# Kernel optimization log

Measured on AMD Instinct MI355X. Metric: run time of the kernel, lower is better.

## Reference

```python
import jax, jax.numpy as jnp
import numpy as np
import math

B, T, D = 2, 2048, 2048
H, HKV = 32, 8
DH = D // H          # 64
G = H // HKV         # 4 query heads per kv head
ROPE_BASE = 10000.0


def _rope_cos_sin(t, dh):
    inv_freq = 1.0 / (ROPE_BASE ** (jnp.arange(0, dh, 2, dtype=jnp.float32) / dh))
    pos = jnp.arange(t, dtype=jnp.float32)
    freqs = pos[:, None] * inv_freq[None, :]          # [T, Dh/2]
    emb = jnp.concatenate([freqs, freqs], axis=-1)    # [T, Dh]
    return jnp.cos(emb), jnp.sin(emb)


def _rotate_half(y):
    y1, y2 = jnp.split(y, 2, axis=-1)
    return jnp.concatenate([-y2, y1], axis=-1)


def _apply_rope(x, cos, sin):  # x: [..., T, Dh]; cos/sin: [T, Dh]
    return x * cos + _rotate_half(x) * sin


def setup_inputs() -> dict:
    key = jax.random.key(0)
    k = jax.random.split(key, 5)
    x = jax.random.normal(k[0], (B, T, D), dtype=jnp.float32)
    Wq = jax.random.normal(k[1], (D, D), dtype=jnp.float32) * 0.02
    Wk = jax.random.normal(k[2], (D, HKV * DH), dtype=jnp.float32) * 0.02
    Wv = jax.random.normal(k[3], (D, HKV * DH), dtype=jnp.float32) * 0.02
    Wo = jax.random.normal(k[4], (D, D), dtype=jnp.float32) * 0.02
    causal = jnp.tril(jnp.ones((T, T), dtype=bool))
    attn_mask = jnp.where(causal, 0.0, -1e9).astype(jnp.float32)[None, None]  # [1,1,T,T]
    return {"x": x, "Wq": Wq, "Wk": Wk, "Wv": Wv, "Wo": Wo, "attn_mask": attn_mask}


def reference(x, Wq, Wk, Wv, Wo, attn_mask):
    Bx, Tx, Dx = x.shape
    # projections (Linear, no bias)
    q = (x @ Wq).reshape(Bx, Tx, H, DH).transpose(0, 2, 1, 3)      # [B,H,T,Dh]
    kk = (x @ Wk).reshape(Bx, Tx, HKV, DH).transpose(0, 2, 1, 3)   # [B,Hkv,T,Dh]
    vv = (x @ Wv).reshape(Bx, Tx, HKV, DH).transpose(0, 2, 1, 3)   # [B,Hkv,T,Dh]
    # RoPE on q and k (offset=0, no kv cache)
    cos, sin = _rope_cos_sin(Tx, DH)
    q = _apply_rope(q, cos, sin)
    kk = _apply_rope(kk, cos, sin)
    # GQA: group query heads so head h uses kv head h // G (matches repeat_interleave)
    qg = q.reshape(Bx, HKV, G, Tx, DH)
    att = jnp.einsum('bkgtd,bksd->bkgts', qg, kk) / math.sqrt(DH)
    att = att + attn_mask[:, :, None]                              # broadcast over groups
    p = jax.nn.softmax(att, axis=-1)
    ctx = jnp.einsum('bkgts,bksd->bkgtd', p, vv)                   # [B,Hkv,G,T,Dh]
    ctx = ctx.reshape(Bx, H, Tx, DH).transpose(0, 2, 1, 3).reshape(Bx, Tx, Dx)
    return ctx @ Wo
```

## Files before the change

kernel.cpp:

```cpp
#include <hip/hip_runtime.h>
#include <hip/hip_bf16.h>


typedef __bf16 bf16_t;
typedef __bf16 bf16x4 __attribute__((ext_vector_type(4)));
typedef __bf16 bf16x8 __attribute__((ext_vector_type(8)));
typedef float f32x4 __attribute__((ext_vector_type(4)));

#define B_ 2
#define T_ 2048
#define D_ 2048
#define H_ 32
#define HKV_ 8
#define DH_ 64

__device__ __forceinline__ float fast_exp2(float x) { return __builtin_amdgcn_exp2f(x); }

__device__ __forceinline__ void gld_lds16(const bf16_t* g, bf16_t* l) {
  __builtin_amdgcn_global_load_lds((const __attribute__((address_space(1))) unsigned int*)g,
                                   (__attribute__((address_space(3))) unsigned int*)l, 16, 0, 0);
}

__global__ __launch_bounds__(256) void cast_f32_bf16(const float* __restrict__ in,
                                                     bf16_t* __restrict__ out, int n) {
  int i = (blockIdx.x * 256 + threadIdx.x) * 8;
  if (i < n) {
    f32x4 a = *(const f32x4*)&in[i];
    f32x4 b = *(const f32x4*)&in[i + 4];
    bf16x8 o;
    o[0] = (bf16_t)a[0]; o[1] = (bf16_t)a[1]; o[2] = (bf16_t)a[2]; o[3] = (bf16_t)a[3];
    o[4] = (bf16_t)b[0]; o[5] = (bf16_t)b[1]; o[6] = (bf16_t)b[2]; o[7] = (bf16_t)b[3];
    *(bf16x8*)&out[i] = o;
  }
}

__global__ __launch_bounds__(256) void transpose_w(const float* __restrict__ W,
                                                   bf16_t* __restrict__ Wt, int K, int N) {
  __shared__ float tile[64][65];
  int n0 = blockIdx.x * 64, k0 = blockIdx.y * 64;
  int tid = threadIdx.x;
  for (int i = tid; i < 4096; i += 256) {
    int r = i >> 6, c = i & 63;
    tile[r][c] = W[(size_t)(k0 + r) * N + n0 + c];
  }
  __syncthreads();
  for (int i = tid; i < 4096; i += 256) {
    int r = i >> 6, c = i & 63;
    Wt[(size_t)(n0 + r) * K + k0 + c] = (bf16_t)tile[c][r];
  }
}

__global__ __launch_bounds__(256) void transpose_wqkv(const float* __restrict__ Wq,
                                                      const float* __restrict__ Wk,
                                                      const float* __restrict__ Wv,
                                                      bf16_t* __restrict__ Wt) {
  __shared__ float tile[64][65];
  int n0 = blockIdx.x * 64, k0 = blockIdx.y * 64;
  const float* W;
  int srcN, col;
  if (n0 < 2048) { W = Wq; srcN = 2048; col = n0; }
  else if (n0 < 2560) { W = Wk; srcN = 512; col = n0 - 2048; }
  else { W = Wv; srcN = 512; col = n0 - 2560; }
  int tid = threadIdx.x;
  for (int i = tid; i < 4096; i += 256) {
    int r = i >> 6, c = i & 63;
    tile[r][c] = W[(size_t)(k0 + r) * srcN + col + c];
  }
  __syncthreads();
  for (int i = tid; i < 4096; i += 256) {
    int r = i >> 6, c = i & 63;
    Wt[(size_t)(n0 + r) * 2048 + k0 + c] = (bf16_t)tile[c][r];
  }
}

template <typename OutT>
__global__ __launch_bounds__(256) void gemm_bt(const bf16_t* __restrict__ A,
                                               const bf16_t* __restrict__ Bt,
                                               OutT* __restrict__ C, int M, int N, int K) {
  __shared__ __align__(16) bf16_t As[2 * 128 * 32];
  __shared__ __align__(16) bf16_t Bs[2 * 128 * 32];
  int tid = threadIdx.x;
  int lane = tid & 63;
  int wave = tid >> 6;
  int l15 = lane & 15;
  int quad = lane >> 4;
  int m0 = blockIdx.y * 128;
  int n0 = blockIdx.x * 128;
  int wrow = (wave >> 1) * 64;
  int wcol = (wave & 1) * 64;

  f32x4 acc[4][4] = {};

  for (int kc = 0; kc < K; kc += 64) {
#pragma unroll
    for (int kk = 0; kk < 2; ++kk) {
#pragma unroll
      for (int c = 0; c < 2; ++c) {
        int linear = c * 256 + tid;
        int r = linear >> 2, seg = linear & 3;
        gld_lds16(&A[(size_t)(m0 + r) * K + kc + kk * 32 + seg * 8],
                  &As[kk * 4096 + (size_t)(c * 256 + wave * 64) * 8]);
        gld_lds16(&Bt[(size_t)(n0 + r) * K + kc + kk * 32 + seg * 8],
                  &Bs[kk * 4096 + (size_t)(c * 256 + wave * 64) * 8]);
      }
    }
    __syncthreads();
#pragma unroll
    for (int kk = 0; kk < 2; ++kk) {
      bf16x8 af[4], bfr[4];
#pragma unroll
      for (int mi = 0; mi < 4; ++mi)
        af[mi] = *(const bf16x8*)&As[kk * 4096 + (wrow + mi * 16 + l15) * 32 + quad * 8];
#pragma unroll
      for (int ni = 0; ni < 4; ++ni)
        bfr[ni] = *(const bf16x8*)&Bs[kk * 4096 + (wcol + ni * 16 + l15) * 32 + quad * 8];
#pragma unroll
      for (int mi = 0; mi < 4; ++mi)
#pragma unroll
        for (int ni = 0; ni < 4; ++ni)
          acc[mi][ni] = __builtin_amdgcn_mfma_f32_16x16x32_bf16(af[mi], bfr[ni], acc[mi][ni], 0, 0, 0);
    }
    __syncthreads();
  }
#pragma unroll
  for (int mi = 0; mi < 4; ++mi) {
#pragma unroll
    for (int ni = 0; ni < 4; ++ni) {
#pragma unroll
      for (int r = 0; r < 4; ++r) {
        int m = m0 + wrow + mi * 16 + quad * 4 + r;
        int n = n0 + wcol + ni * 16 + l15;
        C[(size_t)m * N + n] = (OutT)acc[mi][ni][r];
      }
    }
  }
}

__global__ __launch_bounds__(256) void rope_qk(const bf16_t* __restrict__ qkv,
                                               bf16_t* __restrict__ qr,
                                               bf16_t* __restrict__ kr) {
  int t = blockIdx.x, b = blockIdx.y;
  int tid = threadIdx.x;
  const bf16_t* row = qkv + (size_t)(b * T_ + t) * 3072;
  const float LN1E4_over32 = 9.210340371976184f / 32.0f;
  const float QSC = 1.44269504088896f * 0.125f;
  for (int i = tid; i < 1024 + 256; i += 256) {
    bool isq = i < 1024;
    int ii = isq ? i : i - 1024;
    int hh = ii >> 5, j = ii & 31;
    int base = isq ? 0 : 2048;
    float inv = __expf(-(float)j * LN1E4_over32);
    float fr = (float)t * inv;
    float sn, cs;
    sincosf(fr, &sn, &cs);
    float x1 = (float)row[base + hh * 64 + j];
    float x2 = (float)row[base + hh * 64 + j + 32];
    float o1 = x1 * cs - x2 * sn;
    float o2 = x2 * cs + x1 * sn;
    if (isq) {
      size_t o = ((size_t)(b * H_ + hh) * T_ + t) * DH_;
      qr[o + j] = (bf16_t)(o1 * QSC);
      qr[o + j + 32] = (bf16_t)(o2 * QSC);
    } else {
      size_t o = ((size_t)(b * HKV_ + hh) * T_ + t) * DH_;
      kr[o + j] = (bf16_t)o1;
      kr[o + j + 32] = (bf16_t)o2;
    }
  }
}

__global__ __launch_bounds__(256) void transpose_v(const bf16_t* __restrict__ qkv,
                                                   bf16_t* __restrict__ vtr) {
  __shared__ __align__(16) bf16_t tile[64][72];
  int t0 = blockIdx.x * 64;
  int hk = blockIdx.y;
  int b = blockIdx.z;
  int tid = threadIdx.x;
  for (int i = tid; i < 512; i += 256) {
    int r = i >> 3, s = i & 7;
    *(bf16x8*)&tile[r][s * 8] =
        *(const bf16x8*)&qkv[(size_t)(b * T_ + t0 + r) * 3072 + 2560 + hk * 64 + s * 8];
  }
  __syncthreads();
  for (int i = tid; i < 4096; i += 256) {
    int dd = i >> 6, tt = i & 63;
    vtr[((size_t)(b * HKV_ + hk) * DH_ + dd) * T_ + t0 + tt] = tile[tt][dd];
  }
}

#define DO_HALF(HALF, QF, O, LACC, DOMASK)                                             \
  {                                                                                    \
    f32x4 s_[4] = {};                                                                  \
    _Pragma("unroll") for (int mt = 0; mt < 4; ++mt) {                                 \
      bf16x8 ak0 = *(const bf16x8*)&Ks[(mt * 16 + l15) * 72 + quad * 8];               \
      bf16x8 ak1 = *(const bf16x8*)&Ks[(mt * 16 + l15) * 72 + 32 + quad * 8];          \
      s_[mt] = __builtin_amdgcn_mfma_f32_16x16x32_bf16(ak0, QF[0], s_[mt], 0, 0, 0);   \
      s_[mt] = __builtin_amdgcn_mfma_f32_16x16x32_bf16(ak1, QF[1], s_[mt], 0, 0, 0);   \
    }                                                                                  \
    if (DOMASK) {                                                                      \
      _Pragma("unroll") for (int mt = 0; mt < 4; ++mt)                                 \
          _Pragma("unroll") for (int r = 0; r < 4; ++r) if (mt * 16 + quad * 4 + r >   \
                                                            wave * 16 + l15)           \
              s_[mt][r] = -1e30f;                                                      \
    }                                                                                  \
    _Pragma("unroll") for (int mt = 0; mt < 4; ++mt) {                                 \
      bf16x4 pv;                                                                       \
      _Pragma("unroll") for (int r = 0; r < 4; ++r) {                                  \
        float p = fast_exp2(s_[mt][r]);                                                \
        LACC += p;                                                                     \
        pv[r] = (bf16_t)p;                                                             \
      }                                                                                \
      *(bf16x4*)&Ps[wave][HALF][l15 * 72 + mt * 16 + quad * 4] = pv;                   \
    }                                                                                  \
    _Pragma("unroll") for (int k0 = 0; k0 < 2; ++k0) {                                 \
      bf16x8 ap = *(const bf16x8*)&Ps[wave][HALF][l15 * 72 + k0 * 32 + quad * 8];      \
      _Pragma("unroll") for (int dn = 0; dn < 4; ++dn) {                               \
        bf16x8 bv = *(const bf16x8*)&Vt[(dn * 16 + l15) * 72 + k0 * 32 + quad * 8];    \
        O[dn] = __builtin_amdgcn_mfma_f32_16x16x32_bf16(ap, bv, O[dn], 0, 0, 0);       \
      }                                                                                \
    }                                                                                  \
  }

__global__ __launch_bounds__(256) void flash_attn(const bf16_t* __restrict__ qr,
                                                  const bf16_t* __restrict__ kr,
                                                  const bf16_t* __restrict__ vtr,
                                                  bf16_t* __restrict__ ctxb) {
  __shared__ __align__(16) bf16_t Ks[64 * 72];
  __shared__ __align__(16) bf16_t Vt[64 * 72];
  __shared__ __align__(16) bf16_t Ps[4][2][16 * 72];
  int tid = threadIdx.x;
  int lane = tid & 63;
  int wave = tid >> 6;
  int l15 = lane & 15, quad = lane >> 4;
  int pair = blockIdx.x, h = blockIdx.y, b = blockIdx.z;
  int qtA = pair, qtB = 31 - pair;
  int nkvA = qtA + 1, nkvB = qtB + 1;
  int kvh = h >> 2;

  const bf16_t* qbA = qr + ((size_t)(b * H_ + h) * T_ + qtA * 64 + wave * 16) * DH_;
  const bf16_t* qbB = qr + ((size_t)(b * H_ + h) * T_ + qtB * 64 + wave * 16) * DH_;
  const bf16_t* kbase = kr + (size_t)(b * HKV_ + kvh) * T_ * DH_;
  const bf16_t* vbase = vtr + (size_t)(b * HKV_ + kvh) * DH_ * T_;

  bf16x8 qA[2], qB[2];
#pragma unroll
  for (int k0 = 0; k0 < 2; ++k0) {
    qA[k0] = *(const bf16x8*)&qbA[l15 * 64 + k0 * 32 + quad * 8];
    qB[k0] = *(const bf16x8*)&qbB[l15 * 64 + k0 * 32 + quad * 8];
  }

  f32x4 oA[4] = {}, oB[4] = {};
  float lA = 0.f, lB = 0.f;

  bf16x8 kreg[2], vreg[2];
  auto load_kv = [&](int kv) {
#pragma unroll
    for (int c = 0; c < 2; ++c) {
      int idx = c * 256 + tid;
      int r = idx >> 3, sg = idx & 7;
      kreg[c] = *(const bf16x8*)&kbase[(size_t)kv * 4096 + r * 64 + sg * 8];
      vreg[c] = *(const bf16x8*)&vbase[(size_t)r * T_ + kv * 64 + sg * 8];
    }
  };
  load_kv(0);

  for (int kv = 0; kv < nkvB; ++kv) {
#pragma unroll
    for (int c = 0; c < 2; ++c) {
      int idx = c * 256 + tid;
      int r = idx >> 3, sg = idx & 7;
      *(bf16x8*)&Ks[r * 72 + sg * 8] = kreg[c];
      *(bf16x8*)&Vt[r * 72 + sg * 8] = vreg[c];
    }
    __syncthreads();
    if (kv + 1 < nkvB) load_kv(kv + 1);

    DO_HALF(1, qB, oB, lB, kv == qtB);
    if (kv < nkvA) DO_HALF(0, qA, oA, lA, kv == qtA);
    __syncthreads();
  }

  lA += __shfl_xor(lA, 16, 64);
  lA += __shfl_xor(lA, 32, 64);
  lB += __shfl_xor(lB, 16, 64);
  lB += __shfl_xor(lB, 32, 64);
  float invA = 1.0f / lA, invB = 1.0f / lB;
#pragma unroll
  for (int r = 0; r < 4; ++r) {
    float iAr = __shfl(invA, quad * 4 + r, 64);
    float iBr = __shfl(invB, quad * 4 + r, 64);
    int tA = qtA * 64 + wave * 16 + quad * 4 + r;
    int tB = qtB * 64 + wave * 16 + quad * 4 + r;
#pragma unroll
    for (int dn = 0; dn < 4; ++dn) {
      ctxb[(size_t)(b * T_ + tA) * D_ + h * 64 + dn * 16 + l15] = (bf16_t)(oA[dn][r] * iAr);
      ctxb[(size_t)(b * T_ + tB) * D_ + h * 64 + dn * 16 + l15] = (bf16_t)(oB[dn][r] * iBr);
    }
  }
}

extern "C" void kernel_launch(void* const* d_in, const int* in_sizes, int n_in,
                              void* d_out, int out_size, void* d_ws, size_t ws_size,
                              hipStream_t stream) {
  const float* x = (const float*)d_in[0];
  const float* Wq = (const float*)d_in[1];
  const float* Wk = (const float*)d_in[2];
  const float* Wv = (const float*)d_in[3];
  const float* Wo = (const float*)d_in[4];
  float* out = (float*)d_out;

  char* ws = (char*)d_ws;
  size_t off = 0;
  bf16_t* xb = (bf16_t*)(ws + off); off += (size_t)B_ * T_ * D_ * 2;
  bf16_t* wqkvb = (bf16_t*)(ws + off); off += (size_t)3072 * 2048 * 2;
  bf16_t* wob = (bf16_t*)(ws + off); off += (size_t)2048 * 2048 * 2;
  bf16_t* qkv = (bf16_t*)(ws + off); off += (size_t)4096 * 3072 * 2;
  bf16_t* qr = (bf16_t*)(ws + off); off += (size_t)B_ * H_ * T_ * DH_ * 2;
  bf16_t* kr = (bf16_t*)(ws + off); off += (size_t)B_ * HKV_ * T_ * DH_ * 2;
  bf16_t* vtr = (bf16_t*)(ws + off); off += (size_t)B_ * HKV_ * T_ * DH_ * 2;
  bf16_t* ctxb = (bf16_t*)(ws + off); off += (size_t)B_ * T_ * D_ * 2;

  int nx = B_ * T_ * D_;
  cast_f32_bf16<<<nx / 8 / 256, 256, 0, stream>>>(x, xb, nx);
  transpose_wqkv<<<dim3(3072 / 64, 2048 / 64), 256, 0, stream>>>(Wq, Wk, Wv, wqkvb);
  transpose_w<<<dim3(2048 / 64, 2048 / 64), 256, 0, stream>>>(Wo, wob, 2048, 2048);

  gemm_bt<bf16_t><<<dim3(3072 / 128, 4096 / 128), 256, 0, stream>>>(xb, wqkvb, qkv, 4096, 3072, 2048);

  rope_qk<<<dim3(T_, B_), 256, 0, stream>>>(qkv, qr, kr);
  transpose_v<<<dim3(T_ / 64, HKV_, B_), 256, 0, stream>>>(qkv, vtr);

  flash_attn<<<dim3(16, H_, B_), 256, 0, stream>>>(qr, kr, vtr, ctxb);

  gemm_bt<float><<<dim3(2048 / 128, 4096 / 128), 256, 0, stream>>>(ctxb, wob, out, 4096, 2048, 2048);
}
```

Before: 341.0 us.

## Keep P in registers via permuted V layout and double-buffer K/V LDS

The V transpose now writes keys in a permuted order that matches the MFMA accumulator layout of the score tile. This lets the attention kernel pack exp(S) directly into the A-operand registers for the PV MFMA, with no round trip through LDS. It also double-buffers the K/V shared tiles and drops the trailing barrier in each iteration, so fewer syncs are needed per KV step. The cost is twice the K/V LDS, plus reliance on a single barrier per iteration for correctness across buffers.

Result: faster. 317.3 us (-7.0%).

```diff
diff --git a/kernel.cpp b/kernel.cpp
--- a/kernel.cpp
+++ b/kernel.cpp
@@ -184,16 +184,17 @@
   __syncthreads();
   for (int i = tid; i < 4096; i += 256) {
     int dd = i >> 6, tt = i & 63;
-    vtr[((size_t)(b * HKV_ + hk) * DH_ + dd) * T_ + t0 + tt] = tile[tt][dd];
-  }
-}
-
-#define DO_HALF(HALF, QF, O, LACC, DOMASK)                                             \
+    int src = (tt & 32) | ((tt & 4) << 2) | ((tt & 24) >> 1) | (tt & 3);
+    vtr[((size_t)(b * HKV_ + hk) * DH_ + dd) * T_ + t0 + tt] = tile[src][dd];
+  }
+}
+
+#define DO_HALF(QF, O, LACC, DOMASK, KS, VT)                                           \
   {                                                                                    \
     f32x4 s_[4] = {};                                                                  \
     _Pragma("unroll") for (int mt = 0; mt < 4; ++mt) {                                 \
-      bf16x8 ak0 = *(const bf16x8*)&Ks[(mt * 16 + l15) * 72 + quad * 8];               \
-      bf16x8 ak1 = *(const bf16x8*)&Ks[(mt * 16 + l15) * 72 + 32 + quad * 8];          \
+      bf16x8 ak0 = *(const bf16x8*)&KS[(mt * 16 + l15) * 72 + quad * 8];               \
+      bf16x8 ak1 = *(const bf16x8*)&KS[(mt * 16 + l15) * 72 + 32 + quad * 8];          \
       s_[mt] = __builtin_amdgcn_mfma_f32_16x16x32_bf16(ak0, QF[0], s_[mt], 0, 0, 0);   \
       s_[mt] = __builtin_amdgcn_mfma_f32_16x16x32_bf16(ak1, QF[1], s_[mt], 0, 0, 0);   \
     }                                                                                  \
@@ -203,20 +204,17 @@
                                                             wave * 16 + l15)           \
               s_[mt][r] = -1e30f;                                                      \
     }                                                                                  \
-    _Pragma("unroll") for (int mt = 0; mt < 4; ++mt) {                                 \
-      bf16x4 pv;                                                                       \
-      _Pragma("unroll") for (int r = 0; r < 4; ++r) {                                  \
-        float p = fast_exp2(s_[mt][r]);                                                \
+    _Pragma("unroll") for (int k0 = 0; k0 < 2; ++k0) {                                 \
+      bf16x8 pa;                                                                       \
+      _Pragma("unroll") for (int hh = 0; hh < 2; ++hh)                                 \
+          _Pragma("unroll") for (int r = 0; r < 4; ++r) {                              \
+        float p = fast_exp2(s_[2 * k0 + hh][r]);                                       \
         LACC += p;                                                                     \
-        pv[r] = (bf16_t)p;                                                             \
+        pa[hh * 4 + r] = (bf16_t)p;                                                    \
       }                                                                                \
-      *(bf16x4*)&Ps[wave][HALF][l15 * 72 + mt * 16 + quad * 4] = pv;                   \
-    }                                                                                  \
-    _Pragma("unroll") for (int k0 = 0; k0 < 2; ++k0) {                                 \
-      bf16x8 ap = *(const bf16x8*)&Ps[wave][HALF][l15 * 72 + k0 * 32 + quad * 8];      \
       _Pragma("unroll") for (int dn = 0; dn < 4; ++dn) {                               \
-        bf16x8 bv = *(const bf16x8*)&Vt[(dn * 16 + l15) * 72 + k0 * 32 + quad * 8];    \
-        O[dn] = __builtin_amdgcn_mfma_f32_16x16x32_bf16(ap, bv, O[dn], 0, 0, 0);       \
+        bf16x8 bv = *(const bf16x8*)&VT[(dn * 16 + l15) * 72 + k0 * 32 + quad * 8];    \
+        O[dn] = __builtin_amdgcn_mfma_f32_16x16x32_bf16(pa, bv, O[dn], 0, 0, 0);       \
       }                                                                                \
     }                                                                                  \
   }
@@ -225,9 +223,8 @@
                                                   const bf16_t* __restrict__ kr,
                                                   const bf16_t* __restrict__ vtr,
                                                   bf16_t* __restrict__ ctxb) {
-  __shared__ __align__(16) bf16_t Ks[64 * 72];
-  __shared__ __align__(16) bf16_t Vt[64 * 72];
-  __shared__ __align__(16) bf16_t Ps[4][2][16 * 72];
+  __shared__ __align__(16) bf16_t Ks[2][64 * 72];
+  __shared__ __align__(16) bf16_t Vt[2][64 * 72];
   int tid = threadIdx.x;
   int lane = tid & 63;
   int wave = tid >> 6;
@@ -265,19 +262,20 @@
   load_kv(0);
 
   for (int kv = 0; kv < nkvB; ++kv) {
+    bf16_t* ks = Ks[kv & 1];
+    bf16_t* vt = Vt[kv & 1];
 #pragma unroll
     for (int c = 0; c < 2; ++c) {
       int idx = c * 256 + tid;
       int r = idx >> 3, sg = idx & 7;
-      *(bf16x8*)&Ks[r * 72 + sg * 8] = kreg[c];
-      *(bf16x8*)&Vt[r * 72 + sg * 8] = vreg[c];
+      *(bf16x8*)&ks[r * 72 + sg * 8] = kreg[c];
+      *(bf16x8*)&vt[r * 72 + sg * 8] = vreg[c];
     }
     __syncthreads();
     if (kv + 1 < nkvB) load_kv(kv + 1);
 
-    DO_HALF(1, qB, oB, lB, kv == qtB);
-    if (kv < nkvA) DO_HALF(0, qA, oA, lA, kv == qtA);
-    __syncthreads();
+    DO_HALF(qB, oB, lB, kv == qtB, ks, vt);
+    if (kv < nkvA) DO_HALF(qA, oA, lA, kv == qtA, ks, vt);
   }
 
   lA += __shfl_xor(lA, 16, 64);
```
